# Kernel optimization log

Hardware: AMD Instinct MI355X
Metric: run time of the kernel (lower is better)

The kernel has to match this reference:

```python
import jax, jax.numpy as jnp
import numpy as np

B, L, CIN, COUT, TEMB, N_MODES = 32, 8192, 64, 64, 256, 64
M = N_MODES // 2 + 1  # retained rfft modes = 33
EPS = 1e-5


def setup_inputs() -> dict:
    key = jax.random.key(0)
    ks = jax.random.split(key, 12)
    std_w = float(np.sqrt(1.0 / (2.0 * CIN)))
    # flax Dense default kernel init = lecun_normal ~ normal(std=1/sqrt(fan_in)); plain normal is fine for a reference
    return {
        "x": jax.random.normal(ks[0], (B, L, CIN), jnp.float32),
        "t_emb": jax.random.normal(ks[1], (B, TEMB), jnp.float32),
        # SpectralFreqTimeConv1D params
        "spec_w_real": jax.random.normal(ks[2], (M, CIN, COUT), jnp.float32) * std_w,
        "spec_w_imag": jax.random.normal(ks[3], (M, CIN, COUT), jnp.float32) * std_w,
        "dense_re": jax.random.normal(ks[4], (TEMB, M), jnp.float32) / np.sqrt(TEMB),
        "dense_im": jax.random.normal(ks[5], (TEMB, M), jnp.float32) / np.sqrt(TEMB),
        # TimeConv1D params
        "conv_kernel": jax.random.normal(ks[6], (CIN, COUT), jnp.float32) / np.sqrt(CIN),
        "conv_bias": jnp.zeros((COUT,), jnp.float32),
        "tc_weights": jax.random.normal(ks[7], (COUT, COUT), jnp.float32) * 0.01,  # nn.initializers.normal() stddev=0.01
        "psi_kernel": jax.random.normal(ks[8], (TEMB, 2 * COUT), jnp.float32) / np.sqrt(TEMB),
        # BatchNorm params
        "bn_scale": jnp.ones((COUT,), jnp.float32),
        "bn_bias": jnp.zeros((COUT,), jnp.float32),
    }


def reference(x, t_emb, spec_w_real, spec_w_imag, dense_re, dense_im,
              conv_kernel, conv_bias, tc_weights, psi_kernel, bn_scale, bn_bias):
    b, L_in, _ = x.shape
    n_freq = L_in // 2 + 1

    # ---- SpectralFreqTimeConv1D ----
    x_ft = jnp.fft.rfft(x, axis=-2, norm="forward")            # (b, n_freq, CIN) complex
    t_c = (t_emb @ dense_re) + 1j * (t_emb @ dense_im)         # (b, M) complex
    W = spec_w_real + 1j * spec_w_imag                          # (M, CIN, COUT) complex
    # diagonal-in-mode modulation: equivalent to the eye-based einsum chain
    out_m = t_c[:, :, None] * jnp.einsum("bmi,mio->bmo", x_ft[:, :M, :], W)  # (b, M, COUT)
    out_ft = jnp.zeros((b, n_freq, COUT), jnp.complex64).at[:, :M, :].set(out_m)
    x_spec = jnp.fft.irfft(out_ft, axis=-2, n=L_in, norm="forward")  # (b, L, COUT)

    # ---- TimeConv1D (residual branch) ----
    h = x @ conv_kernel + conv_bias                             # 1x1 conv: (b, L, COUT)
    psi = t_emb @ psi_kernel                                    # (b, 2*COUT)
    w_t, b_t = jnp.split(psi, 2, axis=-1)
    # einsum('ij,bjk,blk->bli', W, diag(w_t), h) == (h * w_t) @ W^T
    x_res = jnp.einsum("blj,ij->bli", h * w_t[:, None, :], tc_weights) + b_t[:, None, :]

    # ---- combine, batchnorm (training: batch stats), activation ----
    out = x_spec + x_res
    mean = out.mean(axis=(0, 1))
    var = out.var(axis=(0, 1))
    out = (out - mean) * jax.lax.rsqrt(var + EPS) * bn_scale + bn_bias
    return jax.nn.relu(out)
```

## Files before the change

### kernel.cpp

```cpp
#include <hip/hip_runtime.h>
#include <hip/hip_fp16.h>

typedef short short8 __attribute__((ext_vector_type(8)));
typedef float f32x4 __attribute__((ext_vector_type(4)));
typedef unsigned int u32;
typedef u32 u32x4 __attribute__((ext_vector_type(4)));
typedef unsigned short u16;

#define BB 32
#define LL 8192
#define TE 256
#define MM 33
#define INVL (1.0f/8192.0f)

#define VTB_OFF  589824
#define DD_OFF   720896
#define DD2_OFF  722944
#define BNP_OFF  731200

#define SRED2_OFF 4227072
#define VF_OFF    4491264

static __device__ __forceinline__ u16 f2b(float f) {
  u32 u = __float_as_uint(f);
  return (u16)((u + 0x7FFFu + ((u >> 16) & 1u)) >> 16);
}
static __device__ __forceinline__ u32 pk2(float lo, float hi) {
  return __builtin_amdgcn_perm(__float_as_uint(hi) + 0x8000u,
                               __float_as_uint(lo) + 0x8000u,
                               0x07060302u);
}
static __device__ __forceinline__ float fsin(float rev) {
  float r; asm("v_sin_f32 %0, %1" : "=v"(r) : "v"(rev)); return r;
}
static __device__ __forceinline__ float fcos(float rev) {
  float r; asm("v_cos_f32 %0, %1" : "=v"(r) : "v"(rev)); return r;
}
static __device__ __forceinline__ u16 tval(int m, bool is_sin, int l) {
  float rev = (float)((m * l) & (LL - 1)) * INVL;
  return f2b(is_sin ? fsin(rev) : fcos(rev));
}
static __device__ __forceinline__ u16 tslotj(int j, int l) {
  int m = (j == 0) ? 32 : (j <= 32 ? j : j - 32);
  bool is_sin = (j == 0) || (j >= 33);
  return tval(m, is_sin, l);
}

__global__ __launch_bounds__(512) void k_dft(const float* __restrict__ x,
                                             float* __restrict__ scr) {
  __shared__ __align__(16) u16 sX[2][64 * 136];
  __shared__ float sOnes[8 * 64];
  int tid = threadIdx.x;
  int b = blockIdx.x >> 5, chunk = blockIdx.x & 31;
  int l0 = chunk * 256;
  int w = tid >> 6, lane = tid & 63;

  f32x4 acc[4];
#pragma unroll
  for (int ct = 0; ct < 4; ++ct) acc[ct] = (f32x4){0.f, 0.f, 0.f, 0.f};

  int arow = lane & 15;
  int kb = (lane >> 4) * 8;
  bool isg = (w >= 4);
  int gi = w - 4;
  int sc = tid & 63, lg = tid >> 6;

  int jrow = w * 16 + arow;
  int m_slot = (jrow == 0) ? 32 : (jrow <= 32 ? jrow : jrow - 32);
  bool is_sin = (jrow == 0) || (jrow >= 33);

  float vx[16];
  float psum = 0.f;
#pragma unroll
  for (int i = 0; i < 16; ++i)
    vx[i] = x[(b * LL + l0 + lg * 16 + i) * 64 + sc];
  {
    u32 wv[8];
#pragma unroll
    for (int j = 0; j < 8; ++j) {
      wv[j] = pk2(vx[2 * j], vx[2 * j + 1]);
      psum += vx[2 * j] + vx[2 * j + 1];
    }
    u32x4* dst = (u32x4*)&sX[0][sc * 136 + lg * 16];
    dst[0] = (u32x4){wv[0], wv[1], wv[2], wv[3]};
    dst[1] = (u32x4){wv[4], wv[5], wv[6], wv[7]};
  }
  __syncthreads();

#pragma unroll
  for (int i = 0; i < 16; ++i)
    vx[i] = x[(b * LL + l0 + 128 + lg * 16 + i) * 64 + sc];

#pragma unroll
  for (int kk = 0; kk < 4; ++kk) {
    short8 a;
    if (isg) {
      a = *reinterpret_cast<const short8*>(&sX[0][(gi * 16 + arow) * 136 + kk * 32 + kb]);
    } else {
      union { short8 s; u32 wv[4]; } A;
      int lb = l0 + kk * 32 + kb;
#pragma unroll
      for (int p2 = 0; p2 < 4; ++p2)
        A.wv[p2] = (u32)tval(m_slot, is_sin, lb + 2 * p2) |
                   ((u32)tval(m_slot, is_sin, lb + 2 * p2 + 1) << 16);
      a = A.s;
    }
#pragma unroll
    for (int ct = 0; ct < 4; ++ct) {
      short8 bf = *reinterpret_cast<const short8*>(&sX[0][(ct * 16 + arow) * 136 + kk * 32 + kb]);
      acc[ct] = __builtin_amdgcn_mfma_f32_16x16x32_bf16(a, bf, acc[ct], 0, 0, 0);
    }
  }

  {
    u32 wv[8];
#pragma unroll
    for (int j = 0; j < 8; ++j) {
      wv[j] = pk2(vx[2 * j], vx[2 * j + 1]);
      psum += vx[2 * j] + vx[2 * j + 1];
    }
    u32x4* dst = (u32x4*)&sX[1][sc * 136 + lg * 16];
    dst[0] = (u32x4){wv[0], wv[1], wv[2], wv[3]};
    dst[1] = (u32x4){wv[4], wv[5], wv[6], wv[7]};
  }
  sOnes[tid] = psum;
  __syncthreads();

#pragma unroll
  for (int kk = 0; kk < 4; ++kk) {
    short8 a;
    if (isg) {
      a = *reinterpret_cast<const short8*>(&sX[1][(gi * 16 + arow) * 136 + kk * 32 + kb]);
    } else {
      union { short8 s; u32 wv[4]; } A;
      int lb = l0 + 128 + kk * 32 + kb;
#pragma unroll
      for (int p2 = 0; p2 < 4; ++p2)
        A.wv[p2] = (u32)tval(m_slot, is_sin, lb + 2 * p2) |
                   ((u32)tval(m_slot, is_sin, lb + 2 * p2 + 1) << 16);
      a = A.s;
    }
#pragma unroll
    for (int ct = 0; ct < 4; ++ct) {
      short8 bf = *reinterpret_cast<const short8*>(&sX[1][(ct * 16 + arow) * 136 + kk * 32 + kb]);
      acc[ct] = __builtin_amdgcn_mfma_f32_16x16x32_bf16(a, bf, acc[ct], 0, 0, 0);
    }
  }

  int rowbase = isg ? (65 + gi * 16) : (w * 16);
  int rowb = (lane >> 4) * 4;
  u16* pp = (u16*)scr + (size_t)(b * 32 + chunk) * 129 * 64;
#pragma unroll
  for (int ct = 0; ct < 4; ++ct) {
    int col = ct * 16 + (lane & 15);
#pragma unroll
    for (int r = 0; r < 4; ++r)
      pp[(rowbase + rowb + r) * 64 + col] = __half_as_ushort(__float2half(acc[ct][r]));
  }
  if (tid < 64) {
    float s = 0.f;
#pragma unroll
    for (int g = 0; g < 8; ++g) s += sOnes[g * 64 + tid];
    pp[64 * 64 + tid] = __half_as_ushort(__float2half(s));
  }
}

__global__ __launch_bounds__(256) void k_red1(float* __restrict__ scr) {
  int bid = blockIdx.x, tid = threadIdx.x;
  int b = bid / 17, rx = bid % 17;
  int p = rx * 256 + tid;
  if (p >= 4128) return;
  const u32* pb = (const u32*)scr + (size_t)b * 32 * 4128;
  float a0 = 0.f, a1 = 0.f;
#pragma unroll 8
  for (int ch = 0; ch < 32; ++ch) {
    u32 u = pb[ch * 4128 + p];
    __half2 h2 = *reinterpret_cast<const __half2*>(&u);
    float2 f = __half22float2(h2);
    a0 += f.x; a1 += f.y;
  }
  *reinterpret_cast<float2*>(scr + SRED2_OFF + b * 8256 + 2 * p) =
      make_float2(a0, a1);
}

__global__ __launch_bounds__(256) void k_vb(
    const float* __restrict__ t_emb, const float* __restrict__ dre,
    const float* __restrict__ dim_, const float* __restrict__ pk,
    const float* __restrict__ swr, const float* __restrict__ swi,
    const float* __restrict__ ck, const float* __restrict__ cbias,
    const float* __restrict__ tw, float* __restrict__ scr,
    float* __restrict__ ws) {
  __shared__ float smem[12352];
  int tid = threadIdx.x;

  if (blockIdx.x < 33) {
    int m = blockIdx.x;
    float2* sW = (float2*)smem;
    float2* sX = (float2*)(smem + 8192);
    float* sTcb = smem + 8192 + 4096;

    for (int idx = tid; idx < 8192; idx += 256) smem[idx] = t_emb[idx];
    __syncthreads();
    if (tid < 64) {
      int b = tid & 31;
      const float* dd = (tid < 32) ? dre : dim_;
      float a = 0.f;
#pragma unroll 8
      for (int j = 0; j < TE; ++j) a = fmaf(smem[b * 256 + j], dd[j * MM + m], a);
      sTcb[tid] = a;
    }
    __syncthreads();

    for (int idx = tid; idx < 4096; idx += 256)
      sW[idx] = make_float2(swr[m * 4096 + idx], swi[m * 4096 + idx]);
    for (int idx = tid; idx < 2048; idx += 256) {
      int b = idx >> 6, i = idx & 63;
      const float* sr = scr + SRED2_OFF + b * 8256;
      float xr, xi;
      if (m == 0)      { xr = sr[64 * 64 + i] * INVL;  xi = 0.f; }
      else if (m < 32) { xr = sr[m * 64 + i] * INVL;   xi = -sr[(32 + m) * 64 + i] * INVL; }
      else             { xr = sr[32 * 64 + i] * INVL;  xi = -sr[0 * 64 + i] * INVL; }
      sX[idx] = make_float2(xr, xi);
    }
    __syncthreads();

    int w = tid >> 6, lane = tid & 63;
    for (int p = 0; p < 8; ++p) {
      int b = p * 4 + w;
      float a0 = 0.f, a1 = 0.f, a2 = 0.f, a3 = 0.f;
#pragma unroll 16
      for (int i = 0; i < 64; ++i) {
        float2 wv = sW[i * 64 + lane];
        float2 xv = sX[b * 64 + i];
        a0 = fmaf(xv.x, wv.x, a0);
        a1 = fmaf(xv.y, wv.y, a1);
        a2 = fmaf(xv.x, wv.y, a2);
        a3 = fmaf(xv.y, wv.x, a3);
      }
      float ar = a0 - a1, ai = a2 + a3;
      float tcr = sTcb[b], tci = sTcb[32 + b];
      float cr = tcr * ar - tci * ai;
      float ci = tcr * ai + tci * ar;
      if (m == 0) {
        ws[DD2_OFF + b * 64 + lane] = cr;
      } else {
        float crr = 2.f * cr, cii = -2.f * ci;
        int js = (m == 32) ? 0 : 32 + m;
        u16* vtb = (u16*)ws + VTB_OFF * 2 + (b * 64 + lane) * 128;
        vtb[64 + m] = f2b(crr);
        vtb[64 + js] = f2b(cii);
        float* vf = scr + VF_OFF + b * 8192;
        vf[(64 + m) * 64 + lane] = crr;
        vf[(64 + js) * 64 + lane] = cii;
      }
    }
  } else {
    int b = blockIdx.x - 33;
    float* sCkT = smem;
    float* sPtw = smem + 4096;
    float* sTe  = smem + 8192;
    float* sPsi = smem + 8448;

    sTe[tid] = t_emb[b * 256 + tid];
    __syncthreads();
    if (tid < 128) {
      float a = 0.f;
#pragma unroll 8
      for (int j = 0; j < TE; ++j) a = fmaf(sTe[j], pk[j * 128 + tid], a);
      sPsi[tid] = a;
    }
    __syncthreads();
    for (int idx = tid; idx < 4096; idx += 256) {
      int c = idx >> 6, j = idx & 63;
      sCkT[j * 64 + c] = ck[idx];
      sPtw[idx] = sPsi[j] * tw[idx];
    }
    __syncthreads();

    u16* vtb = (u16*)ws + VTB_OFF * 2 + b * 64 * 128;
    float* vf = scr + VF_OFF + b * 8192;
    int lane = tid & 63, w = tid >> 6;
#pragma unroll 4
    for (int it = 0; it < 16; ++it) {
      int o = it * 4 + w;
      float a = 0.f;
#pragma unroll 16
      for (int j = 0; j < 64; ++j)
        a = fmaf(sCkT[j * 64 + lane], sPtw[o * 64 + j], a);
      vtb[o * 128 + lane] = f2b(a);
      vf[lane * 64 + o] = a;
    }
    if (tid < 64) {
      float a = 0.f;
      for (int j = 0; j < 64; ++j) a = fmaf(cbias[j], sPtw[tid * 64 + j], a);
      ws[DD_OFF + b * 64 + tid] = a + sPsi[64 + tid];
    }
  }
}

__global__ __launch_bounds__(256) void k_bn(const float* __restrict__ scr,
                                            float* __restrict__ ws) {
  __shared__ float sVx[64 * 64];
  __shared__ float sGx[64 * 64];
  __shared__ float sS[64 * 64];
  __shared__ float sSum[64];
  __shared__ float sP[4][2][64];
  int tid = threadIdx.x, b = blockIdx.x;
  const float* sr = scr + SRED2_OFF + b * 8256;
  const float* vf = scr + VF_OFF + b * 8192;

  for (int p = tid; p < 4096; p += 256) {
    sVx[p] = vf[p];
    sGx[p] = sr[65 * 64 + p];
    sS[p]  = sr[p];
  }
  if (tid < 64) sSum[tid] = sr[64 * 64 + tid];
  __syncthreads();

  int o = tid & 63, part = tid >> 6;
  float m1 = 0.f, q1 = 0.f, cross = 0.f, vt2 = 0.f;
  for (int ii = 0; ii < 16; ++ii) {
    int i = part * 16 + ii;
    float vx = sVx[i * 64 + o];
    m1 = fmaf(sSum[i], vx, m1);
    float w0 = 0.f, w1 = 0.f, c0 = 0.f, c1 = 0.f;
#pragma unroll
    for (int j = 0; j < 64; j += 2) {
      float va = sVx[j * 64 + o], vb = sVx[(j + 1) * 64 + o];
      w0 = fmaf(sGx[i * 64 + j], va, w0);
      w1 = fmaf(sGx[i * 64 + j + 1], vb, w1);
      c0 = fmaf(sS[i * 64 + j], va, c0);
      c1 = fmaf(sS[i * 64 + j + 1], vb, c1);
    }
    q1 = fmaf(vx, w0 + w1, q1);
    float vt = vf[(64 + i) * 64 + o];
    vt2 = fmaf(vt, vt, vt2);
    cross = fmaf(vt, c0 + c1, cross);
  }
  sP[part][0][o] = m1;
  sP[part][1][o] = q1 + 2.f * cross + 4096.f * vt2;
  __syncthreads();
  if (tid < 64) {
    float m = sP[0][0][tid] + sP[1][0][tid] + sP[2][0][tid] + sP[3][0][tid];
    float q = sP[0][1][tid] + sP[1][1][tid] + sP[2][1][tid] + sP[3][1][tid];
    float D = ws[DD_OFF + b * 64 + tid] + ws[DD2_OFF + b * 64 + tid];
    ws[BNP_OFF + b * 128 + tid]      = m + 8192.f * D;
    ws[BNP_OFF + b * 128 + 64 + tid] = q + 2.f * D * m + 8192.f * D * D;
  }
}

__global__ __launch_bounds__(256) void k_main(const float* __restrict__ x,
                                              const float* __restrict__ ws,
                                              const float* __restrict__ bns,
                                              const float* __restrict__ bnb,
                                              float* __restrict__ out) {
  __shared__ float sD[64];
  __shared__ float sA[64];
  __shared__ float sB[64];
  __shared__ float sPp[4][64];
  __shared__ float sPq[4][64];
  int tid = threadIdx.x, w = tid >> 6, lane = tid & 63;
  int b = blockIdx.x >> 6, rg = blockIdx.x & 63;
  const u16* wsu = (const u16*)ws;

  int kb = (lane >> 4) * 8;
  const u16* vtb = wsu + VTB_OFF * 2 + b * 64 * 128;
  short8 bf[4][4];
#pragma unroll
  for (int kk = 0; kk < 4; ++kk)
#pragma unroll
    for (int ct = 0; ct < 4; ++ct)
      bf[kk][ct] = *reinterpret_cast<const short8*>(
          vtb + (ct * 16 + (lane & 15)) * 128 + kk * 32 + kb);

  {
    int o = tid & 63, g = tid >> 6;
    float pm = 0.f, pq = 0.f;
#pragma unroll
    for (int r = 0; r < 8; ++r) {
      int bb = g * 8 + r;
      pm += ws[BNP_OFF + bb * 128 + o];
      pq += ws[BNP_OFF + bb * 128 + 64 + o];
    }
    sPp[g][o] = pm;
    sPq[g][o] = pq;
  }
  if (tid < 64) sD[tid] = ws[DD_OFF + b * 64 + tid] + ws[DD2_OFF + b * 64 + tid];
  __syncthreads();
  if (tid < 64) {
    const float inv_n = 1.f / (32.f * 8192.f);
    float mean = (sPp[0][tid] + sPp[1][tid] + sPp[2][tid] + sPp[3][tid]) * inv_n;
    float ex2  = (sPq[0][tid] + sPq[1][tid] + sPq[2][tid] + sPq[3][tid]) * inv_n;
    float var = ex2 - mean * mean;
    float istd = rsqrtf(var + 1e-5f);
    float al = istd * bns[tid];
    sA[tid] = al;
    sB[tid] = bnb[tid] - mean * al;
  }
  __syncthreads();

  int rowb = (lane >> 4) * 4;
  int lbase = rg * 128 + w * 32;

#pragma unroll
  for (int rt = 0; rt < 2; ++rt) {
    int l = lbase + rt * 16 + (lane & 15);
    const float* xq = x + (b * LL + l) * 64;
    float4 u0 = *reinterpret_cast<const float4*>(xq + kb);
    float4 u1 = *reinterpret_cast<const float4*>(xq + kb + 4);
    float4 u2 = *reinterpret_cast<const float4*>(xq + 32 + kb);
    float4 u3 = *reinterpret_cast<const float4*>(xq + 32 + kb + 4);
    union { short8 s; u32 wv[4]; } A0, A1, A2, A3;
    A0.wv[0] = pk2(u0.x, u0.y); A0.wv[1] = pk2(u0.z, u0.w);
    A0.wv[2] = pk2(u1.x, u1.y); A0.wv[3] = pk2(u1.z, u1.w);
    A1.wv[0] = pk2(u2.x, u2.y); A1.wv[1] = pk2(u2.z, u2.w);
    A1.wv[2] = pk2(u3.x, u3.y); A1.wv[3] = pk2(u3.z, u3.w);
#pragma unroll
    for (int p2 = 0; p2 < 4; ++p2) {
      A2.wv[p2] = (u32)tslotj(kb + 2 * p2, l) |
                  ((u32)tslotj(kb + 2 * p2 + 1, l) << 16);
      A3.wv[p2] = (u32)tslotj(32 + kb + 2 * p2, l) |
                  ((u32)tslotj(32 + kb + 2 * p2 + 1, l) << 16);
    }

    f32x4 acc[4];
#pragma unroll
    for (int ct = 0; ct < 4; ++ct) acc[ct] = (f32x4){0.f, 0.f, 0.f, 0.f};
#pragma unroll
    for (int ct = 0; ct < 4; ++ct) {
      acc[ct] = __builtin_amdgcn_mfma_f32_16x16x32_bf16(A0.s, bf[0][ct], acc[ct], 0, 0, 0);
      acc[ct] = __builtin_amdgcn_mfma_f32_16x16x32_bf16(A1.s, bf[1][ct], acc[ct], 0, 0, 0);
      acc[ct] = __builtin_amdgcn_mfma_f32_16x16x32_bf16(A2.s, bf[2][ct], acc[ct], 0, 0, 0);
      acc[ct] = __builtin_amdgcn_mfma_f32_16x16x32_bf16(A3.s, bf[3][ct], acc[ct], 0, 0, 0);
    }
#pragma unroll
    for (int ct = 0; ct < 4; ++ct) {
      int o = ct * 16 + (lane & 15);
      float dd = sD[o], al = sA[o], be = sB[o];
#pragma unroll
      for (int r = 0; r < 4; ++r) {
        float v = acc[ct][r] + dd;
        out[(b * LL + lbase + rt * 16 + rowb + r) * 64 + o] =
            fmaxf(fmaf(v, al, be), 0.f);
      }
    }
  }
}

extern "C" void kernel_launch(void* const* d_in, const int* in_sizes, int n_in,
                              void* d_out, int out_size, void* d_ws, size_t ws_size,
                              hipStream_t stream) {
  const float* x     = (const float*)d_in[0];
  const float* t_emb = (const float*)d_in[1];
  const float* swr   = (const float*)d_in[2];
  const float* swi   = (const float*)d_in[3];
  const float* dre   = (const float*)d_in[4];
  const float* dim_  = (const float*)d_in[5];
  const float* ck    = (const float*)d_in[6];
  const float* cbias = (const float*)d_in[7];
  const float* tw    = (const float*)d_in[8];
  const float* pk    = (const float*)d_in[9];
  const float* bns   = (const float*)d_in[10];
  const float* bnb   = (const float*)d_in[11];
  float* ws  = (float*)d_ws;
  float* out = (float*)d_out;

  k_dft<<<1024, 512, 0, stream>>>(x, out);
  k_red1<<<544, 256, 0, stream>>>(out);
  k_vb<<<65, 256, 0, stream>>>(t_emb, dre, dim_, pk, swr, swi,
                               ck, cbias, tw, out, ws);
  k_bn<<<32, 256, 0, stream>>>(out, ws);
  k_main<<<2048, 256, 0, stream>>>(x, ws, bns, bnb, out);
}
```

Before: 90.66 us.

## Fold residual weight prep into DFT kernel and merge spectral mix with BN stats

The per-batch residual-weight computation (psi, conv kernel times tc weights) now runs as 32 extra blocks appended to the DFT launch, so it overlaps with the DFT work. The spectral mode mixing and the batchnorm statistics are merged into one per-batch kernel of 1024 threads, which keeps the spectral outputs in shared memory instead of going through global scratch. This removes two launches and one global round-trip. The cost is that each mid block recomputes t_c and rereads the full spectral weights per batch, and only 32 blocks run that stage.

```diff
diff --git a/kernel.cpp b/kernel.cpp
--- a/kernel.cpp
+++ b/kernel.cpp
@@ -46,122 +46,171 @@
   return tval(m, is_sin, l);
 }
 
-__global__ __launch_bounds__(512) void k_dft(const float* __restrict__ x,
-                                             float* __restrict__ scr) {
-  __shared__ __align__(16) u16 sX[2][64 * 136];
-  __shared__ float sOnes[8 * 64];
+__global__ __launch_bounds__(512) void k_dft(
+    const float* __restrict__ x, const float* __restrict__ t_emb,
+    const float* __restrict__ pk, const float* __restrict__ ck,
+    const float* __restrict__ cbias, const float* __restrict__ tw,
+    float* __restrict__ scr, float* __restrict__ ws) {
+  __shared__ __align__(16) unsigned char smraw[36864];
   int tid = threadIdx.x;
-  int b = blockIdx.x >> 5, chunk = blockIdx.x & 31;
-  int l0 = chunk * 256;
-  int w = tid >> 6, lane = tid & 63;
-
-  f32x4 acc[4];
-#pragma unroll
-  for (int ct = 0; ct < 4; ++ct) acc[ct] = (f32x4){0.f, 0.f, 0.f, 0.f};
-
-  int arow = lane & 15;
-  int kb = (lane >> 4) * 8;
-  bool isg = (w >= 4);
-  int gi = w - 4;
-  int sc = tid & 63, lg = tid >> 6;
-
-  int jrow = w * 16 + arow;
-  int m_slot = (jrow == 0) ? 32 : (jrow <= 32 ? jrow : jrow - 32);
-  bool is_sin = (jrow == 0) || (jrow >= 33);
-
-  float vx[16];
-  float psum = 0.f;
-#pragma unroll
-  for (int i = 0; i < 16; ++i)
-    vx[i] = x[(b * LL + l0 + lg * 16 + i) * 64 + sc];
-  {
-    u32 wv[8];
-#pragma unroll
-    for (int j = 0; j < 8; ++j) {
-      wv[j] = pk2(vx[2 * j], vx[2 * j + 1]);
-      psum += vx[2 * j] + vx[2 * j + 1];
-    }
-    u32x4* dst = (u32x4*)&sX[0][sc * 136 + lg * 16];
-    dst[0] = (u32x4){wv[0], wv[1], wv[2], wv[3]};
-    dst[1] = (u32x4){wv[4], wv[5], wv[6], wv[7]};
-  }
-  __syncthreads();
-
-#pragma unroll
-  for (int i = 0; i < 16; ++i)
-    vx[i] = x[(b * LL + l0 + 128 + lg * 16 + i) * 64 + sc];
-
-#pragma unroll
-  for (int kk = 0; kk < 4; ++kk) {
-    short8 a;
-    if (isg) {
-      a = *reinterpret_cast<const short8*>(&sX[0][(gi * 16 + arow) * 136 + kk * 32 + kb]);
-    } else {
-      union { short8 s; u32 wv[4]; } A;
-      int lb = l0 + kk * 32 + kb;
-#pragma unroll
-      for (int p2 = 0; p2 < 4; ++p2)
-        A.wv[p2] = (u32)tval(m_slot, is_sin, lb + 2 * p2) |
-                   ((u32)tval(m_slot, is_sin, lb + 2 * p2 + 1) << 16);
-      a = A.s;
-    }
+
+  if (blockIdx.x < 1024) {
+    u16* sX0 = (u16*)smraw;
+    u16* sX1 = (u16*)smraw + 64 * 136;
+    float* sOnes = (float*)(smraw + 34816);
+    int b = blockIdx.x >> 5, chunk = blockIdx.x & 31;
+    int l0 = chunk * 256;
+    int w = tid >> 6, lane = tid & 63;
+
+    f32x4 acc[4];
+#pragma unroll
+    for (int ct = 0; ct < 4; ++ct) acc[ct] = (f32x4){0.f, 0.f, 0.f, 0.f};
+
+    int arow = lane & 15;
+    int kb = (lane >> 4) * 8;
+    bool isg = (w >= 4);
+    int gi = w - 4;
+    int sc = tid & 63, lg = tid >> 6;
+
+    int jrow = w * 16 + arow;
+    int m_slot = (jrow == 0) ? 32 : (jrow <= 32 ? jrow : jrow - 32);
+    bool is_sin = (jrow == 0) || (jrow >= 33);
+
+    float vx[16];
+    float psum = 0.f;
+#pragma unroll
+    for (int i = 0; i < 16; ++i)
+      vx[i] = x[(b * LL + l0 + lg * 16 + i) * 64 + sc];
+    {
+      u32 wv[8];
+#pragma unroll
+      for (int j = 0; j < 8; ++j) {
+        wv[j] = pk2(vx[2 * j], vx[2 * j + 1]);
+        psum += vx[2 * j] + vx[2 * j + 1];
+      }
+      u32x4* dst = (u32x4*)&sX0[sc * 136 + lg * 16];
+      dst[0] = (u32x4){wv[0], wv[1], wv[2], wv[3]};
+      dst[1] = (u32x4){wv[4], wv[5], wv[6], wv[7]};
+    }
+    __syncthreads();
+
+#pragma unroll
+    for (int i = 0; i < 16; ++i)
+      vx[i] = x[(b * LL + l0 + 128 + lg * 16 + i) * 64 + sc];
+
+#pragma unroll
+    for (int kk = 0; kk < 4; ++kk) {
+      short8 a;
+      if (isg) {
+        a = *reinterpret_cast<const short8*>(&sX0[(gi * 16 + arow) * 136 + kk * 32 + kb]);
+      } else {
+        union { short8 s; u32 wv[4]; } A;
+        int lb = l0 + kk * 32 + kb;
+#pragma unroll
+        for (int p2 = 0; p2 < 4; ++p2)
+          A.wv[p2] = (u32)tval(m_slot, is_sin, lb + 2 * p2) |
+                     ((u32)tval(m_slot, is_sin, lb + 2 * p2 + 1) << 16);
+        a = A.s;
+      }
+#pragma unroll
+      for (int ct = 0; ct < 4; ++ct) {
+        short8 bf = *reinterpret_cast<const short8*>(&sX0[(ct * 16 + arow) * 136 + kk * 32 + kb]);
+        acc[ct] = __builtin_amdgcn_mfma_f32_16x16x32_bf16(a, bf, acc[ct], 0, 0, 0);
+      }
+    }
+
+    {
+      u32 wv[8];
+#pragma unroll
+      for (int j = 0; j < 8; ++j) {
+        wv[j] = pk2(vx[2 * j], vx[2 * j + 1]);
+        psum += vx[2 * j] + vx[2 * j + 1];
+      }
+      u32x4* dst = (u32x4*)&sX1[sc * 136 + lg * 16];
+      dst[0] = (u32x4){wv[0], wv[1], wv[2], wv[3]};
+      dst[1] = (u32x4){wv[4], wv[5], wv[6], wv[7]};
+    }
+    sOnes[tid] = psum;
+    __syncthreads();
+
+#pragma unroll
+    for (int kk = 0; kk < 4; ++kk) {
+      short8 a;
+      if (isg) {
+        a = *reinterpret_cast<const short8*>(&sX1[(gi * 16 + arow) * 136 + kk * 32 + kb]);
+      } else {
+        union { short8 s; u32 wv[4]; } A;
+        int lb = l0 + 128 + kk * 32 + kb;
+#pragma unroll
+        for (int p2 = 0; p2 < 4; ++p2)
+          A.wv[p2] = (u32)tval(m_slot, is_sin, lb + 2 * p2) |
+                     ((u32)tval(m_slot, is_sin, lb + 2 * p2 + 1) << 16);
+        a = A.s;
+      }
+#pragma unroll
+      for (int ct = 0; ct < 4; ++ct) {
+        short8 bf = *reinterpret_cast<const short8*>(&sX1[(ct * 16 + arow) * 136 + kk * 32 + kb]);
+        acc[ct] = __builtin_amdgcn_mfma_f32_16x16x32_bf16(a, bf, acc[ct], 0, 0, 0);
+      }
+    }
+
+    int rowbase = isg ? (65 + gi * 16) : (w * 16);
+    int rowb = (lane >> 4) * 4;
+    u16* pp = (u16*)scr + (size_t)(b * 32 + chunk) * 129 * 64;
 #pragma unroll
     for (int ct = 0; ct < 4; ++ct) {
-      short8 bf = *reinterpret_cast<const short8*>(&sX[0][(ct * 16 + arow) * 136 + kk * 32 + kb]);
-      acc[ct] = __builtin_amdgcn_mfma_f32_16x16x32_bf16(a, bf, acc[ct], 0, 0, 0);
-    }
-  }
-
-  {
-    u32 wv[8];
-#pragma unroll
-    for (int j = 0; j < 8; ++j) {
-      wv[j] = pk2(vx[2 * j], vx[2 * j + 1]);
-      psum += vx[2 * j] + vx[2 * j + 1];
-    }
-    u32x4* dst = (u32x4*)&sX[1][sc * 136 + lg * 16];
-    dst[0] = (u32x4){wv[0], wv[1], wv[2], wv[3]};
-    dst[1] = (u32x4){wv[4], wv[5], wv[6], wv[7]};
-  }
-  sOnes[tid] = psum;
-  __syncthreads();
-
-#pragma unroll
-  for (int kk = 0; kk < 4; ++kk) {
-    short8 a;
-    if (isg) {
-      a = *reinterpret_cast<const short8*>(&sX[1][(gi * 16 + arow) * 136 + kk * 32 + kb]);
-    } else {
-      union { short8 s; u32 wv[4]; } A;
-      int lb = l0 + 128 + kk * 32 + kb;
-#pragma unroll
-      for (int p2 = 0; p2 < 4; ++p2)
-        A.wv[p2] = (u32)tval(m_slot, is_sin, lb + 2 * p2) |
-                   ((u32)tval(m_slot, is_sin, lb + 2 * p2 + 1) << 16);
-      a = A.s;
-    }
-#pragma unroll
-    for (int ct = 0; ct < 4; ++ct) {
-      short8 bf = *reinterpret_cast<const short8*>(&sX[1][(ct * 16 + arow) * 136 + kk * 32 + kb]);
-      acc[ct] = __builtin_amdgcn_mfma_f32_16x16x32_bf16(a, bf, acc[ct], 0, 0, 0);
-    }
-  }
-
-  int rowbase = isg ? (65 + gi * 16) : (w * 16);
-  int rowb = (lane >> 4) * 4;
-  u16* pp = (u16*)scr + (size_t)(b * 32 + chunk) * 129 * 64;
-#pragma unroll
-  for (int ct = 0; ct < 4; ++ct) {
-    int col = ct * 16 + (lane & 15);
-#pragma unroll
-    for (int r = 0; r < 4; ++r)
-      pp[(rowbase + rowb + r) * 64 + col] = __half_as_ushort(__float2half(acc[ct][r]));
-  }
-  if (tid < 64) {
-    float s = 0.f;
-#pragma unroll
-    for (int g = 0; g < 8; ++g) s += sOnes[g * 64 + tid];
-    pp[64 * 64 + tid] = __half_as_ushort(__float2half(s));
+      int col = ct * 16 + (lane & 15);
+#pragma unroll
+      for (int r = 0; r < 4; ++r)
+        pp[(rowbase + rowb + r) * 64 + col] = __half_as_ushort(__float2half(acc[ct][r]));
+    }
+    if (tid < 64) {
+      float s = 0.f;
+#pragma unroll
+      for (int g = 0; g < 8; ++g) s += sOnes[g * 64 + tid];
+      pp[64 * 64 + tid] = __half_as_ushort(__float2half(s));
+    }
+  } else {
+    int b = blockIdx.x - 1024;
+    float* sCkT = (float*)smraw;
+    float* sPtw = (float*)(smraw + 16384);
+    float* sTe  = (float*)(smraw + 32768);
+    float* sPsi = (float*)(smraw + 33792);
+
+    if (tid < 256) sTe[tid] = t_emb[b * 256 + tid];
+    __syncthreads();
+    if (tid < 128) {
+      float a = 0.f;
+#pragma unroll 8
+      for (int j = 0; j < TE; ++j) a = fmaf(sTe[j], pk[j * 128 + tid], a);
+      sPsi[tid] = a;
+    }
+    __syncthreads();
+    for (int idx = tid; idx < 4096; idx += 512) {
+      int c = idx >> 6, j = idx & 63;
+      sCkT[j * 64 + c] = ck[idx];
+      sPtw[idx] = sPsi[j] * tw[idx];
+    }
+    __syncthreads();
+
+    u16* vtb = (u16*)ws + VTB_OFF * 2 + b * 64 * 128;
+    float* vfb = scr + VF_OFF + b * 4096;
+    int lane = tid & 63, w = tid >> 6;
+#pragma unroll 2
+    for (int it = 0; it < 8; ++it) {
+      int o = it * 8 + w;
+      float a = 0.f;
+#pragma unroll 16
+      for (int j = 0; j < 64; ++j)
+        a = fmaf(sCkT[j * 64 + lane], sPtw[o * 64 + j], a);
+      vtb[o * 128 + lane] = f2b(a);
+      vfb[lane * 64 + o] = a;
+    }
+    if (tid < 64) {
+      float a = 0.f;
+      for (int j = 0; j < 64; ++j) a = fmaf(cbias[j], sPtw[tid * 64 + j], a);
+      ws[DD_OFF + b * 64 + tid] = a + sPsi[64 + tid];
+    }
   }
 }
 
@@ -183,146 +232,83 @@
       make_float2(a0, a1);
 }
 
-__global__ __launch_bounds__(256) void k_vb(
+__global__ __launch_bounds__(1024) void k_mid(
     const float* __restrict__ t_emb, const float* __restrict__ dre,
-    const float* __restrict__ dim_, const float* __restrict__ pk,
-    const float* __restrict__ swr, const float* __restrict__ swi,
-    const float* __restrict__ ck, const float* __restrict__ cbias,
-    const float* __restrict__ tw, float* __restrict__ scr,
+    const float* __restrict__ dim_, const float* __restrict__ swr,
+    const float* __restrict__ swi, float* __restrict__ scr,
     float* __restrict__ ws) {
-  __shared__ float smem[12352];
-  int tid = threadIdx.x;
-
-  if (blockIdx.x < 33) {
-    int m = blockIdx.x;
-    float2* sW = (float2*)smem;
-    float2* sX = (float2*)(smem + 8192);
-    float* sTcb = smem + 8192 + 4096;
-
-    for (int idx = tid; idx < 8192; idx += 256) smem[idx] = t_emb[idx];
-    __syncthreads();
-    if (tid < 64) {
-      int b = tid & 31;
-      const float* dd = (tid < 32) ? dre : dim_;
-      float a = 0.f;
-#pragma unroll 8
-      for (int j = 0; j < TE; ++j) a = fmaf(smem[b * 256 + j], dd[j * MM + m], a);
-      sTcb[tid] = a;
-    }
-    __syncthreads();
-
-    for (int idx = tid; idx < 4096; idx += 256)
-      sW[idx] = make_float2(swr[m * 4096 + idx], swi[m * 4096 + idx]);
-    for (int idx = tid; idx < 2048; idx += 256) {
-      int b = idx >> 6, i = idx & 63;
-      const float* sr = scr + SRED2_OFF + b * 8256;
-      float xr, xi;
-      if (m == 0)      { xr = sr[64 * 64 + i] * INVL;  xi = 0.f; }
-      else if (m < 32) { xr = sr[m * 64 + i] * INVL;   xi = -sr[(32 + m) * 64 + i] * INVL; }
-      else             { xr = sr[32 * 64 + i] * INVL;  xi = -sr[0 * 64 + i] * INVL; }
-      sX[idx] = make_float2(xr, xi);
-    }
-    __syncthreads();
-
-    int w = tid >> 6, lane = tid & 63;
-    for (int p = 0; p < 8; ++p) {
-      int b = p * 4 + w;
-      float a0 = 0.f, a1 = 0.f, a2 = 0.f, a3 = 0.f;
-#pragma unroll 16
-      for (int i = 0; i < 64; ++i) {
-        float2 wv = sW[i * 64 + lane];
-        float2 xv = sX[b * 64 + i];
-        a0 = fmaf(xv.x, wv.x, a0);
-        a1 = fmaf(xv.y, wv.y, a1);
-        a2 = fmaf(xv.x, wv.y, a2);
-        a3 = fmaf(xv.y, wv.x, a3);
-      }
-      float ar = a0 - a1, ai = a2 + a3;
-      float tcr = sTcb[b], tci = sTcb[32 + b];
-      float cr = tcr * ar - tci * ai;
-      float ci = tcr * ai + tci * ar;
-      if (m == 0) {
-        ws[DD2_OFF + b * 64 + lane] = cr;
-      } else {
-        float crr = 2.f * cr, cii = -2.f * ci;
-        int js = (m == 32) ? 0 : 32 + m;
-        u16* vtb = (u16*)ws + VTB_OFF * 2 + (b * 64 + lane) * 128;
-        vtb[64 + m] = f2b(crr);
-        vtb[64 + js] = f2b(cii);
-        float* vf = scr + VF_OFF + b * 8192;
-        vf[(64 + m) * 64 + lane] = crr;
-        vf[(64 + js) * 64 + lane] = cii;
-      }
-    }
-  } else {
-    int b = blockIdx.x - 33;
-    float* sCkT = smem;
-    float* sPtw = smem + 4096;
-    float* sTe  = smem + 8192;
-    float* sPsi = smem + 8448;
-
-    sTe[tid] = t_emb[b * 256 + tid];
-    __syncthreads();
-    if (tid < 128) {
-      float a = 0.f;
-#pragma unroll 8
-      for (int j = 0; j < TE; ++j) a = fmaf(sTe[j], pk[j * 128 + tid], a);
-      sPsi[tid] = a;
-    }
-    __syncthreads();
-    for (int idx = tid; idx < 4096; idx += 256) {
-      int c = idx >> 6, j = idx & 63;
-      sCkT[j * 64 + c] = ck[idx];
-      sPtw[idx] = sPsi[j] * tw[idx];
-    }
-    __syncthreads();
-
-    u16* vtb = (u16*)ws + VTB_OFF * 2 + b * 64 * 128;
-    float* vf = scr + VF_OFF + b * 8192;
-    int lane = tid & 63, w = tid >> 6;
-#pragma unroll 4
-    for (int it = 0; it < 16; ++it) {
-      int o = it * 4 + w;
-      float a = 0.f;
-#pragma unroll 16
-      for (int j = 0; j < 64; ++j)
-        a = fmaf(sCkT[j * 64 + lane], sPtw[o * 64 + j], a);
-      vtb[o * 128 + lane] = f2b(a);
-      vf[lane * 64 + o] = a;
-    }
-    if (tid < 64) {
-      float a = 0.f;
-      for (int j = 0; j < 64; ++j) a = fmaf(cbias[j], sPtw[tid * 64 + j], a);
-      ws[DD_OFF + b * 64 + tid] = a + sPsi[64 + tid];
-    }
-  }
-}
-
-__global__ __launch_bounds__(256) void k_bn(const float* __restrict__ scr,
-                                            float* __restrict__ ws) {
+  __shared__ float sS[65 * 64];
   __shared__ float sVx[64 * 64];
+  __shared__ float sVt[64 * 64];
   __shared__ float sGx[64 * 64];
-  __shared__ float sS[64 * 64];
-  __shared__ float sSum[64];
-  __shared__ float sP[4][2][64];
+  __shared__ float sT[TE];
+  __shared__ float sTcr[MM], sTci[MM];
+  __shared__ float sCr0[64];
+  __shared__ float sP[16][2][64];
   int tid = threadIdx.x, b = blockIdx.x;
   const float* sr = scr + SRED2_OFF + b * 8256;
-  const float* vf = scr + VF_OFF + b * 8192;
-
-  for (int p = tid; p < 4096; p += 256) {
-    sVx[p] = vf[p];
+  const float* vfb = scr + VF_OFF + b * 4096;
+
+  for (int p = tid; p < 4160; p += 1024) sS[p] = sr[p];
+  for (int p = tid; p < 4096; p += 1024) {
+    sVx[p] = vfb[p];
     sGx[p] = sr[65 * 64 + p];
-    sS[p]  = sr[p];
-  }
-  if (tid < 64) sSum[tid] = sr[64 * 64 + tid];
-  __syncthreads();
-
-  int o = tid & 63, part = tid >> 6;
+  }
+  if (tid < 256) sT[tid] = t_emb[b * 256 + tid];
+  __syncthreads();
+  if (tid < 66) {
+    int m = (tid < 33) ? tid : tid - 33;
+    const float* dd = (tid < 33) ? dre : dim_;
+    float a = 0.f;
+#pragma unroll 8
+    for (int j = 0; j < TE; ++j) a = fmaf(sT[j], dd[j * MM + m], a);
+    if (tid < 33) sTcr[m] = a; else sTci[m] = a;
+  }
+  __syncthreads();
+
+  int w = tid >> 6, o = tid & 63;
+  for (int q = 0; q < 3; ++q) {
+    int m = w + 16 * q;
+    if (m > 32) break;
+    int rr = (m == 0) ? 64 : (m < 32 ? m : 32);
+    int ri = (m == 0) ? -1 : (m < 32 ? 32 + m : 0);
+    const float* wrp = swr + m * 4096 + o;
+    const float* wip = swi + m * 4096 + o;
+    float a0 = 0.f, a1 = 0.f, a2 = 0.f, a3 = 0.f;
+#pragma unroll 8
+    for (int i = 0; i < 64; ++i) {
+      float xr = sS[rr * 64 + i] * INVL;
+      float xi = (ri < 0) ? 0.f : -sS[ri * 64 + i] * INVL;
+      float wr = wrp[i * 64], wi = wip[i * 64];
+      a0 = fmaf(xr, wr, a0);
+      a1 = fmaf(xi, wi, a1);
+      a2 = fmaf(xr, wi, a2);
+      a3 = fmaf(xi, wr, a3);
+    }
+    float ar = a0 - a1, ai = a2 + a3;
+    float cr = sTcr[m] * ar - sTci[m] * ai;
+    float ci = sTcr[m] * ai + sTci[m] * ar;
+    if (m == 0) {
+      sCr0[o] = cr;
+      ws[DD2_OFF + b * 64 + o] = cr;
+    } else {
+      float crr = 2.f * cr, cii = -2.f * ci;
+      int js = (m == 32) ? 0 : 32 + m;
+      u16* vtb = (u16*)ws + VTB_OFF * 2 + (b * 64 + o) * 128;
+      vtb[64 + m] = f2b(crr);
+      vtb[64 + js] = f2b(cii);
+      sVt[m * 64 + o] = crr;
+      sVt[js * 64 + o] = cii;
+    }
+  }
+  __syncthreads();
+
+  int part = tid >> 6;
   float m1 = 0.f, q1 = 0.f, cross = 0.f, vt2 = 0.f;
-  for (int ii = 0; ii < 16; ++ii) {
-    int i = part * 16 + ii;
+  for (int ii = 0; ii < 4; ++ii) {
+    int i = part * 4 + ii;
     float vx = sVx[i * 64 + o];
-    m1 = fmaf(sSum[i], vx, m1);
+    m1 = fmaf(sS[64 * 64 + i], vx, m1);
     float w0 = 0.f, w1 = 0.f, c0 = 0.f, c1 = 0.f;
 #pragma unroll
     for (int j = 0; j < 64; j += 2) {
@@ -333,7 +319,7 @@
       c1 = fmaf(sS[i * 64 + j + 1], vb, c1);
     }
     q1 = fmaf(vx, w0 + w1, q1);
-    float vt = vf[(64 + i) * 64 + o];
+    float vt = sVt[i * 64 + o];
     vt2 = fmaf(vt, vt, vt2);
     cross = fmaf(vt, c0 + c1, cross);
   }
@@ -341,9 +327,10 @@
   sP[part][1][o] = q1 + 2.f * cross + 4096.f * vt2;
   __syncthreads();
   if (tid < 64) {
-    float m = sP[0][0][tid] + sP[1][0][tid] + sP[2][0][tid] + sP[3][0][tid];
-    float q = sP[0][1][tid] + sP[1][1][tid] + sP[2][1][tid] + sP[3][1][tid];
-    float D = ws[DD_OFF + b * 64 + tid] + ws[DD2_OFF + b * 64 + tid];
+    float m = 0.f, q = 0.f;
+#pragma unroll
+    for (int p = 0; p < 16; ++p) { m += sP[p][0][tid]; q += sP[p][1][tid]; }
+    float D = ws[DD_OFF + b * 64 + tid] + sCr0[tid];
     ws[BNP_OFF + b * 128 + tid]      = m + 8192.f * D;
     ws[BNP_OFF + b * 128 + 64 + tid] = q + 2.f * D * m + 8192.f * D * D;
   }
@@ -465,10 +452,8 @@
   float* ws  = (float*)d_ws;
   float* out = (float*)d_out;
 
-  k_dft<<<1024, 512, 0, stream>>>(x, out);
+  k_dft<<<1056, 512, 0, stream>>>(x, t_emb, pk, ck, cbias, tw, out, ws);
   k_red1<<<544, 256, 0, stream>>>(out);
-  k_vb<<<65, 256, 0, stream>>>(t_emb, dre, dim_, pk, swr, swi,
-                               ck, cbias, tw, out, ws);
-  k_bn<<<32, 256, 0, stream>>>(out, ws);
+  k_mid<<<32, 1024, 0, stream>>>(t_emb, dre, dim_, swr, swi, out, ws);
   k_main<<<2048, 256, 0, stream>>>(x, ws, bns, bnb, out);
 }
```

After: 112.0 us. 23.5% more time.

## Merge small setup kernels into DFT and reduction launches to cut launch count

Applied to the files above, without the earlier changes.

The per-batch residual-weight blocks of k_vb now run as 32 extra blocks of k_dft, and the chunk reduction (k_red1) plus the per-mode spectral mixing run together in a new k_rv kernel. The mode blocks no longer wait for the reduced sums. They re-sum the 32 half-precision chunk partials directly for their own rows. This removes one kernel launch and one serialization point, at the cost of redundant reads of the partials by the 33 mode blocks and a larger shared-memory footprint for the DFT blocks.

```diff
diff --git a/kernel.cpp b/kernel.cpp
--- a/kernel.cpp
+++ b/kernel.cpp
@@ -25,6 +25,9 @@
   u32 u = __float_as_uint(f);
   return (u16)((u + 0x7FFFu + ((u >> 16) & 1u)) >> 16);
 }
+static __device__ __forceinline__ float h2f(u16 v) {
+  __half_raw hr; hr.x = v; return __half2float(__half(hr));
+}
 static __device__ __forceinline__ u32 pk2(float lo, float hi) {
   return __builtin_amdgcn_perm(__float_as_uint(hi) + 0x8000u,
                                __float_as_uint(lo) + 0x8000u,
@@ -46,222 +49,138 @@
   return tval(m, is_sin, l);
 }
 
-__global__ __launch_bounds__(512) void k_dft(const float* __restrict__ x,
-                                             float* __restrict__ scr) {
-  __shared__ __align__(16) u16 sX[2][64 * 136];
-  __shared__ float sOnes[8 * 64];
+__global__ __launch_bounds__(512) void k_dft(
+    const float* __restrict__ x, const float* __restrict__ t_emb,
+    const float* __restrict__ pk, const float* __restrict__ ck,
+    const float* __restrict__ cbias, const float* __restrict__ tw,
+    float* __restrict__ scr, float* __restrict__ ws) {
+  __shared__ __align__(16) unsigned char smraw[36864];
   int tid = threadIdx.x;
-  int b = blockIdx.x >> 5, chunk = blockIdx.x & 31;
-  int l0 = chunk * 256;
-  int w = tid >> 6, lane = tid & 63;
-
-  f32x4 acc[4];
-#pragma unroll
-  for (int ct = 0; ct < 4; ++ct) acc[ct] = (f32x4){0.f, 0.f, 0.f, 0.f};
-
-  int arow = lane & 15;
-  int kb = (lane >> 4) * 8;
-  bool isg = (w >= 4);
-  int gi = w - 4;
-  int sc = tid & 63, lg = tid >> 6;
-
-  int jrow = w * 16 + arow;
-  int m_slot = (jrow == 0) ? 32 : (jrow <= 32 ? jrow : jrow - 32);
-  bool is_sin = (jrow == 0) || (jrow >= 33);
-
-  float vx[16];
-  float psum = 0.f;
-#pragma unroll
-  for (int i = 0; i < 16; ++i)
-    vx[i] = x[(b * LL + l0 + lg * 16 + i) * 64 + sc];
-  {
-    u32 wv[8];
-#pragma unroll
-    for (int j = 0; j < 8; ++j) {
-      wv[j] = pk2(vx[2 * j], vx[2 * j + 1]);
-      psum += vx[2 * j] + vx[2 * j + 1];
-    }
-    u32x4* dst = (u32x4*)&sX[0][sc * 136 + lg * 16];
-    dst[0] = (u32x4){wv[0], wv[1], wv[2], wv[3]};
-    dst[1] = (u32x4){wv[4], wv[5], wv[6], wv[7]};
-  }
-  __syncthreads();
-
-#pragma unroll
-  for (int i = 0; i < 16; ++i)
-    vx[i] = x[(b * LL + l0 + 128 + lg * 16 + i) * 64 + sc];
-
-#pragma unroll
-  for (int kk = 0; kk < 4; ++kk) {
-    short8 a;
-    if (isg) {
-      a = *reinterpret_cast<const short8*>(&sX[0][(gi * 16 + arow) * 136 + kk * 32 + kb]);
-    } else {
-      union { short8 s; u32 wv[4]; } A;
-      int lb = l0 + kk * 32 + kb;
-#pragma unroll
-      for (int p2 = 0; p2 < 4; ++p2)
-        A.wv[p2] = (u32)tval(m_slot, is_sin, lb + 2 * p2) |
-                   ((u32)tval(m_slot, is_sin, lb + 2 * p2 + 1) << 16);
-      a = A.s;
-    }
+
+  if (blockIdx.x < 1024) {
+    u16* sX0 = (u16*)smraw;
+    u16* sX1 = (u16*)smraw + 64 * 136;
+    float* sOnes = (float*)(smraw + 34816);
+    int b = blockIdx.x >> 5, chunk = blockIdx.x & 31;
+    int l0 = chunk * 256;
+    int w = tid >> 6, lane = tid & 63;
+
+    f32x4 acc[4];
+#pragma unroll
+    for (int ct = 0; ct < 4; ++ct) acc[ct] = (f32x4){0.f, 0.f, 0.f, 0.f};
+
+    int arow = lane & 15;
+    int kb = (lane >> 4) * 8;
+    bool isg = (w >= 4);
+    int gi = w - 4;
+    int sc = tid & 63, lg = tid >> 6;
+
+    int jrow = w * 16 + arow;
+    int m_slot = (jrow == 0) ? 32 : (jrow <= 32 ? jrow : jrow - 32);
+    bool is_sin = (jrow == 0) || (jrow >= 33);
+
+    float vx[16];
+    float psum = 0.f;
+#pragma unroll
+    for (int i = 0; i < 16; ++i)
+      vx[i] = x[(b * LL + l0 + lg * 16 + i) * 64 + sc];
+    {
+      u32 wv[8];
+#pragma unroll
+      for (int j = 0; j < 8; ++j) {
+        wv[j] = pk2(vx[2 * j], vx[2 * j + 1]);
+        psum += vx[2 * j] + vx[2 * j + 1];
+      }
+      u32x4* dst = (u32x4*)&sX0[sc * 136 + lg * 16];
+      dst[0] = (u32x4){wv[0], wv[1], wv[2], wv[3]};
+      dst[1] = (u32x4){wv[4], wv[5], wv[6], wv[7]};
+    }
+    __syncthreads();
+
+#pragma unroll
+    for (int i = 0; i < 16; ++i)
+      vx[i] = x[(b * LL + l0 + 128 + lg * 16 + i) * 64 + sc];
+
+#pragma unroll
+    for (int kk = 0; kk < 4; ++kk) {
+      short8 a;
+      if (isg) {
+        a = *reinterpret_cast<const short8*>(&sX0[(gi * 16 + arow) * 136 + kk * 32 + kb]);
+      } else {
+        union { short8 s; u32 wv[4]; } A;
+        int lb = l0 + kk * 32 + kb;
+#pragma unroll
+        for (int p2 = 0; p2 < 4; ++p2)
+          A.wv[p2] = (u32)tval(m_slot, is_sin, lb + 2 * p2) |
+                     ((u32)tval(m_slot, is_sin, lb + 2 * p2 + 1) << 16);
+        a = A.s;
+      }
+#pragma unroll
+      for (int ct = 0; ct < 4; ++ct) {
+        short8 bf = *reinterpret_cast<const short8*>(&sX0[(ct * 16 + arow) * 136 + kk * 32 + kb]);
+        acc[ct] = __builtin_amdgcn_mfma_f32_16x16x32_bf16(a, bf, acc[ct], 0, 0, 0);
+      }
+    }
+
+    {
+      u32 wv[8];
+#pragma unroll
+      for (int j = 0; j < 8; ++j) {
+        wv[j] = pk2(vx[2 * j], vx[2 * j + 1]);
+        psum += vx[2 * j] + vx[2 * j + 1];
+      }
+      u32x4* dst = (u32x4*)&sX1[sc * 136 + lg * 16];
+      dst[0] = (u32x4){wv[0], wv[1], wv[2], wv[3]};
+      dst[1] = (u32x4){wv[4], wv[5], wv[6], wv[7]};
+    }
+    sOnes[tid] = psum;
+    __syncthreads();
+
+#pragma unroll
+    for (int kk = 0; kk < 4; ++kk) {
+      short8 a;
+      if (isg) {
+        a = *reinterpret_cast<const short8*>(&sX1[(gi * 16 + arow) * 136 + kk * 32 + kb]);
+      } else {
+        union { short8 s; u32 wv[4]; } A;
+        int lb = l0 + 128 + kk * 32 + kb;
+#pragma unroll
+        for (int p2 = 0; p2 < 4; ++p2)
+          A.wv[p2] = (u32)tval(m_slot, is_sin, lb + 2 * p2) |
+                     ((u32)tval(m_slot, is_sin, lb + 2 * p2 + 1) << 16);
+        a = A.s;
+      }
+#pragma unroll
+      for (int ct = 0; ct < 4; ++ct) {
+        short8 bf = *reinterpret_cast<const short8*>(&sX1[(ct * 16 + arow) * 136 + kk * 32 + kb]);
+        acc[ct] = __builtin_amdgcn_mfma_f32_16x16x32_bf16(a, bf, acc[ct], 0, 0, 0);
+      }
+    }
+
+    int rowbase = isg ? (65 + gi * 16) : (w * 16);
+    int rowb = (lane >> 4) * 4;
+    u16* pp = (u16*)scr + (size_t)(b * 32 + chunk) * 129 * 64;
 #pragma unroll
     for (int ct = 0; ct < 4; ++ct) {
-      short8 bf = *reinterpret_cast<const short8*>(&sX[0][(ct * 16 + arow) * 136 + kk * 32 + kb]);
-      acc[ct] = __builtin_amdgcn_mfma_f32_16x16x32_bf16(a, bf, acc[ct], 0, 0, 0);
-    }
-  }
-
-  {
-    u32 wv[8];
-#pragma unroll
-    for (int j = 0; j < 8; ++j) {
-      wv[j] = pk2(vx[2 * j], vx[2 * j + 1]);
-      psum += vx[2 * j] + vx[2 * j + 1];
-    }
-    u32x4* dst = (u32x4*)&sX[1][sc * 136 + lg * 16];
-    dst[0] = (u32x4){wv[0], wv[1], wv[2], wv[3]};
-    dst[1] = (u32x4){wv[4], wv[5], wv[6], wv[7]};
-  }
-  sOnes[tid] = psum;
-  __syncthreads();
-
-#pragma unroll
-  for (int kk = 0; kk < 4; ++kk) {
-    short8 a;
-    if (isg) {
-      a = *reinterpret_cast<const short8*>(&sX[1][(gi * 16 + arow) * 136 + kk * 32 + kb]);
-    } else {
-      union { short8 s; u32 wv[4]; } A;
-      int lb = l0 + 128 + kk * 32 + kb;
-#pragma unroll
-      for (int p2 = 0; p2 < 4; ++p2)
-        A.wv[p2] = (u32)tval(m_slot, is_sin, lb + 2 * p2) |
-                   ((u32)tval(m_slot, is_sin, lb + 2 * p2 + 1) << 16);
-      a = A.s;
-    }
-#pragma unroll
-    for (int ct = 0; ct < 4; ++ct) {
-      short8 bf = *reinterpret_cast<const short8*>(&sX[1][(ct * 16 + arow) * 136 + kk * 32 + kb]);
-      acc[ct] = __builtin_amdgcn_mfma_f32_16x16x32_bf16(a, bf, acc[ct], 0, 0, 0);
-    }
-  }
-
-  int rowbase = isg ? (65 + gi * 16) : (w * 16);
-  int rowb = (lane >> 4) * 4;
-  u16* pp = (u16*)scr + (size_t)(b * 32 + chunk) * 129 * 64;
-#pragma unroll
-  for (int ct = 0; ct < 4; ++ct) {
-    int col = ct * 16 + (lane & 15);
-#pragma unroll
-    for (int r = 0; r < 4; ++r)
-      pp[(rowbase + rowb + r) * 64 + col] = __half_as_ushort(__float2half(acc[ct][r]));
-  }
-  if (tid < 64) {
-    float s = 0.f;
-#pragma unroll
-    for (int g = 0; g < 8; ++g) s += sOnes[g * 64 + tid];
-    pp[64 * 64 + tid] = __half_as_ushort(__float2half(s));
-  }
-}
-
-__global__ __launch_bounds__(256) void k_red1(float* __restrict__ scr) {
-  int bid = blockIdx.x, tid = threadIdx.x;
-  int b = bid / 17, rx = bid % 17;
-  int p = rx * 256 + tid;
-  if (p >= 4128) return;
-  const u32* pb = (const u32*)scr + (size_t)b * 32 * 4128;
-  float a0 = 0.f, a1 = 0.f;
-#pragma unroll 8
-  for (int ch = 0; ch < 32; ++ch) {
-    u32 u = pb[ch * 4128 + p];
-    __half2 h2 = *reinterpret_cast<const __half2*>(&u);
-    float2 f = __half22float2(h2);
-    a0 += f.x; a1 += f.y;
-  }
-  *reinterpret_cast<float2*>(scr + SRED2_OFF + b * 8256 + 2 * p) =
-      make_float2(a0, a1);
-}
-
-__global__ __launch_bounds__(256) void k_vb(
-    const float* __restrict__ t_emb, const float* __restrict__ dre,
-    const float* __restrict__ dim_, const float* __restrict__ pk,
-    const float* __restrict__ swr, const float* __restrict__ swi,
-    const float* __restrict__ ck, const float* __restrict__ cbias,
-    const float* __restrict__ tw, float* __restrict__ scr,
-    float* __restrict__ ws) {
-  __shared__ float smem[12352];
-  int tid = threadIdx.x;
-
-  if (blockIdx.x < 33) {
-    int m = blockIdx.x;
-    float2* sW = (float2*)smem;
-    float2* sX = (float2*)(smem + 8192);
-    float* sTcb = smem + 8192 + 4096;
-
-    for (int idx = tid; idx < 8192; idx += 256) smem[idx] = t_emb[idx];
-    __syncthreads();
+      int col = ct * 16 + (lane & 15);
+#pragma unroll
+      for (int r = 0; r < 4; ++r)
+        pp[(rowbase + rowb + r) * 64 + col] = __half_as_ushort(__float2half(acc[ct][r]));
+    }
     if (tid < 64) {
-      int b = tid & 31;
-      const float* dd = (tid < 32) ? dre : dim_;
-      float a = 0.f;
-#pragma unroll 8
-      for (int j = 0; j < TE; ++j) a = fmaf(smem[b * 256 + j], dd[j * MM + m], a);
-      sTcb[tid] = a;
-    }
-    __syncthreads();
-
-    for (int idx = tid; idx < 4096; idx += 256)
-      sW[idx] = make_float2(swr[m * 4096 + idx], swi[m * 4096 + idx]);
-    for (int idx = tid; idx < 2048; idx += 256) {
-      int b = idx >> 6, i = idx & 63;
-      const float* sr = scr + SRED2_OFF + b * 8256;
-      float xr, xi;
-      if (m == 0)      { xr = sr[64 * 64 + i] * INVL;  xi = 0.f; }
-      else if (m < 32) { xr = sr[m * 64 + i] * INVL;   xi = -sr[(32 + m) * 64 + i] * INVL; }
-      else             { xr = sr[32 * 64 + i] * INVL;  xi = -sr[0 * 64 + i] * INVL; }
-      sX[idx] = make_float2(xr, xi);
-    }
-    __syncthreads();
-
-    int w = tid >> 6, lane = tid & 63;
-    for (int p = 0; p < 8; ++p) {
-      int b = p * 4 + w;
-      float a0 = 0.f, a1 = 0.f, a2 = 0.f, a3 = 0.f;
-#pragma unroll 16
-      for (int i = 0; i < 64; ++i) {
-        float2 wv = sW[i * 64 + lane];
-        float2 xv = sX[b * 64 + i];
-        a0 = fmaf(xv.x, wv.x, a0);
-        a1 = fmaf(xv.y, wv.y, a1);
-        a2 = fmaf(xv.x, wv.y, a2);
-        a3 = fmaf(xv.y, wv.x, a3);
-      }
-      float ar = a0 - a1, ai = a2 + a3;
-      float tcr = sTcb[b], tci = sTcb[32 + b];
-      float cr = tcr * ar - tci * ai;
-      float ci = tcr * ai + tci * ar;
-      if (m == 0) {
-        ws[DD2_OFF + b * 64 + lane] = cr;
-      } else {
-        float crr = 2.f * cr, cii = -2.f * ci;
-        int js = (m == 32) ? 0 : 32 + m;
-        u16* vtb = (u16*)ws + VTB_OFF * 2 + (b * 64 + lane) * 128;
-        vtb[64 + m] = f2b(crr);
-        vtb[64 + js] = f2b(cii);
-        float* vf = scr + VF_OFF + b * 8192;
-        vf[(64 + m) * 64 + lane] = crr;
-        vf[(64 + js) * 64 + lane] = cii;
-      }
+      float s = 0.f;
+#pragma unroll
+      for (int g = 0; g < 8; ++g) s += sOnes[g * 64 + tid];
+      pp[64 * 64 + tid] = __half_as_ushort(__float2half(s));
     }
   } else {
-    int b = blockIdx.x - 33;
-    float* sCkT = smem;
-    float* sPtw = smem + 4096;
-    float* sTe  = smem + 8192;
-    float* sPsi = smem + 8448;
-
-    sTe[tid] = t_emb[b * 256 + tid];
+    int b = blockIdx.x - 1024;
+    float* sCkT = (float*)smraw;
+    float* sPtw = (float*)(smraw + 16384);
+    float* sTe  = (float*)(smraw + 32768);
+    float* sPsi = (float*)(smraw + 33792);
+
+    if (tid < 256) sTe[tid] = t_emb[b * 256 + tid];
     __syncthreads();
     if (tid < 128) {
       float a = 0.f;
@@ -270,7 +189,7 @@
       sPsi[tid] = a;
     }
     __syncthreads();
-    for (int idx = tid; idx < 4096; idx += 256) {
+    for (int idx = tid; idx < 4096; idx += 512) {
       int c = idx >> 6, j = idx & 63;
       sCkT[j * 64 + c] = ck[idx];
       sPtw[idx] = sPsi[j] * tw[idx];
@@ -280,9 +199,9 @@
     u16* vtb = (u16*)ws + VTB_OFF * 2 + b * 64 * 128;
     float* vf = scr + VF_OFF + b * 8192;
     int lane = tid & 63, w = tid >> 6;
-#pragma unroll 4
-    for (int it = 0; it < 16; ++it) {
-      int o = it * 4 + w;
+#pragma unroll 2
+    for (int it = 0; it < 8; ++it) {
+      int o = it * 8 + w;
       float a = 0.f;
 #pragma unroll 16
       for (int j = 0; j < 64; ++j)
@@ -294,6 +213,100 @@
       float a = 0.f;
       for (int j = 0; j < 64; ++j) a = fmaf(cbias[j], sPtw[tid * 64 + j], a);
       ws[DD_OFF + b * 64 + tid] = a + sPsi[64 + tid];
+    }
+  }
+}
+
+__global__ __launch_bounds__(256) void k_rv(
+    const float* __restrict__ t_emb, const float* __restrict__ dre,
+    const float* __restrict__ dim_, const float* __restrict__ swr,
+    const float* __restrict__ swi, float* __restrict__ scr,
+    float* __restrict__ ws) {
+  __shared__ float smem[12352];
+  int bid = blockIdx.x, tid = threadIdx.x;
+
+  if (bid < 544) {
+    int b = bid / 17, rx = bid % 17;
+    int p = rx * 256 + tid;
+    if (p >= 4128) return;
+    const u32* pb = (const u32*)scr + (size_t)b * 32 * 4128;
+    float a0 = 0.f, a1 = 0.f;
+#pragma unroll 8
+    for (int ch = 0; ch < 32; ++ch) {
+      u32 u = pb[ch * 4128 + p];
+      __half2 hh = *reinterpret_cast<const __half2*>(&u);
+      float2 f = __half22float2(hh);
+      a0 += f.x; a1 += f.y;
+    }
+    *reinterpret_cast<float2*>(scr + SRED2_OFF + b * 8256 + 2 * p) =
+        make_float2(a0, a1);
+    return;
+  }
+
+  int m = bid - 544;
+  float2* sW = (float2*)smem;
+  float2* sX = (float2*)(smem + 8192);
+  float* sTcb = smem + 8192 + 4096;
+
+  for (int idx = tid; idx < 8192; idx += 256) smem[idx] = t_emb[idx];
+  __syncthreads();
+  if (tid < 64) {
+    int b = tid & 31;
+    const float* dd = (tid < 32) ? dre : dim_;
+    float a = 0.f;
+#pragma unroll 8
+    for (int j = 0; j < TE; ++j) a = fmaf(smem[b * 256 + j], dd[j * MM + m], a);
+    sTcb[tid] = a;
+  }
+  __syncthreads();
+
+  for (int idx = tid; idx < 4096; idx += 256)
+    sW[idx] = make_float2(swr[m * 4096 + idx], swi[m * 4096 + idx]);
+  {
+    int rr = (m == 0) ? 64 : (m < 32 ? m : 32);
+    int ri = (m == 0) ? -1 : (m < 32 ? 32 + m : 0);
+    for (int idx = tid; idx < 2048; idx += 256) {
+      int b = idx >> 6, i = idx & 63;
+      const u16* pb = (const u16*)scr + (size_t)b * 32 * 8256;
+      float xr = 0.f, xi = 0.f;
+#pragma unroll 8
+      for (int ch = 0; ch < 32; ++ch) {
+        xr += h2f(pb[ch * 8256 + rr * 64 + i]);
+        if (ri >= 0) xi -= h2f(pb[ch * 8256 + ri * 64 + i]);
+      }
+      sX[idx] = make_float2(xr * INVL, xi * INVL);
+    }
+  }
+  __syncthreads();
+
+  int w = tid >> 6, lane = tid & 63;
+  for (int p = 0; p < 8; ++p) {
+    int b = p * 4 + w;
+    float a0 = 0.f, a1 = 0.f, a2 = 0.f, a3 = 0.f;
+#pragma unroll 16
+    for (int i = 0; i < 64; ++i) {
+      float2 wv = sW[i * 64 + lane];
+      float2 xv = sX[b * 64 + i];
+      a0 = fmaf(xv.x, wv.x, a0);
+      a1 = fmaf(xv.y, wv.y, a1);
+      a2 = fmaf(xv.x, wv.y, a2);
+      a3 = fmaf(xv.y, wv.x, a3);
+    }
+    float ar = a0 - a1, ai = a2 + a3;
+    float tcr = sTcb[b], tci = sTcb[32 + b];
+    float cr = tcr * ar - tci * ai;
+    float ci = tcr * ai + tci * ar;
+    if (m == 0) {
+      ws[DD2_OFF + b * 64 + lane] = cr;
+    } else {
+      float crr = 2.f * cr, cii = -2.f * ci;
+      int js = (m == 32) ? 0 : 32 + m;
+      u16* vtb = (u16*)ws + VTB_OFF * 2 + (b * 64 + lane) * 128;
+      vtb[64 + m] = f2b(crr);
+      vtb[64 + js] = f2b(cii);
+      float* vf = scr + VF_OFF + b * 8192;
+      vf[(64 + m) * 64 + lane] = crr;
+      vf[(64 + js) * 64 + lane] = cii;
     }
   }
 }
@@ -465,10 +478,8 @@
   float* ws  = (float*)d_ws;
   float* out = (float*)d_out;
 
-  k_dft<<<1024, 512, 0, stream>>>(x, out);
-  k_red1<<<544, 256, 0, stream>>>(out);
-  k_vb<<<65, 256, 0, stream>>>(t_emb, dre, dim_, pk, swr, swi,
-                               ck, cbias, tw, out, ws);
+  k_dft<<<1056, 512, 0, stream>>>(x, t_emb, pk, ck, cbias, tw, out, ws);
+  k_rv<<<577, 256, 0, stream>>>(t_emb, dre, dim_, swr, swi, out, ws);
   k_bn<<<32, 256, 0, stream>>>(out, ws);
   k_main<<<2048, 256, 0, stream>>>(x, ws, bns, bnb, out);
 }
```

Result: slower. 178.6 us (+97.1%).
